# Kernel tuning notes

Measured on AMD Instinct MI355X. Metric: run time of the kernel, lower is better.

## Reference

```python
import jax, jax.numpy as jnp
import numpy as np

B, T, D = 8, 2048, 1024
FF = 4 * D
EPS = 1e-5


def setup_inputs() -> dict:
    key = jax.random.key(0)
    ks = jax.random.split(key, 20)
    rn = lambda k, s, sc=0.02: (jax.random.normal(k, s, jnp.float32) * sc)
    return {
        "x": jax.random.normal(ks[0], (B, T, D), jnp.float32),
        "ln1_g": jnp.ones((D,), jnp.float32),
        "ln1_b": jnp.zeros((D,), jnp.float32),
        "ln2_g": jnp.ones((D,), jnp.float32),
        "ln2_b": jnp.zeros((D,), jnp.float32),
        # time-mixing lerp coefficients in [0,1]
        "tm_mix_k": jax.random.uniform(ks[1], (D,), jnp.float32),
        "tm_mix_v": jax.random.uniform(ks[2], (D,), jnp.float32),
        "tm_mix_r": jax.random.uniform(ks[3], (D,), jnp.float32),
        # per-channel decay (log-log space, w = -exp(time_decay)) and first-token bonus
        "time_decay": rn(ks[4], (D,), 1.0),
        "time_first": rn(ks[5], (D,), 0.5),
        "wk": rn(ks[6], (D, D)),
        "wv": rn(ks[7], (D, D)),
        "wr": rn(ks[8], (D, D)),
        "wo": rn(ks[9], (D, D)),
        "cm_mix_k": jax.random.uniform(ks[10], (D,), jnp.float32),
        "cm_mix_r": jax.random.uniform(ks[11], (D,), jnp.float32),
        "cwk": rn(ks[12], (D, FF)),
        "cwv": rn(ks[13], (FF, D)),
        "cwr": rn(ks[14], (D, D)),
    }


def layer_norm(x, g, b):
    mu = jnp.mean(x, axis=-1, keepdims=True)
    var = jnp.var(x, axis=-1, keepdims=True)
    return (x - mu) * jax.lax.rsqrt(var + EPS) * g + b


def token_shift(x):
    # x[:, t-1] with zeros at t=0 (fresh state)
    return jnp.pad(x, ((0, 0), (1, 0), (0, 0)))[:, :-1]


def wkv_scan(k, v, time_decay, time_first):
    """Numerically-stable RWKV-4 WKV linear recurrence. k,v: [B,T,D]."""
    w = -jnp.exp(time_decay)  # [D], negative log-decay per step
    u = time_first

    def step(carry, kv):
        aa, bb, pp = carry  # each [B, D]
        kt, vt = kv
        ww = u + kt
        p = jnp.maximum(pp, ww)
        e1 = jnp.exp(pp - p)
        e2 = jnp.exp(ww - p)
        out = (e1 * aa + e2 * vt) / (e1 * bb + e2)
        ww2 = pp + w
        p2 = jnp.maximum(ww2, kt)
        e1b = jnp.exp(ww2 - p2)
        e2b = jnp.exp(kt - p2)
        return (e1b * aa + e2b * vt, e1b * bb + e2b, p2), out

    z = jnp.zeros((k.shape[0], k.shape[2]), k.dtype)
    init = (z, z, jnp.full_like(z, -1e38))
    _, outs = jax.lax.scan(step, init, (jnp.moveaxis(k, 1, 0), jnp.moveaxis(v, 1, 0)))
    return jnp.moveaxis(outs, 0, 1)  # [B,T,D]


def reference(x, ln1_g, ln1_b, ln2_g, ln2_b,
              tm_mix_k, tm_mix_v, tm_mix_r, time_decay, time_first,
              wk, wv, wr, wo, cm_mix_k, cm_mix_r, cwk, cwv, cwr):
    # --- Time mixing (pre-LN residual) ---
    h = layer_norm(x, ln1_g, ln1_b)
    hx = token_shift(h)
    k = jnp.einsum("btd,de->bte", h * tm_mix_k + hx * (1.0 - tm_mix_k), wk)
    v = jnp.einsum("btd,de->bte", h * tm_mix_v + hx * (1.0 - tm_mix_v), wv)
    r = jax.nn.sigmoid(jnp.einsum("btd,de->bte", h * tm_mix_r + hx * (1.0 - tm_mix_r), wr))
    wkv = wkv_scan(k, v, time_decay, time_first)
    x = x + jnp.einsum("btd,de->bte", r * wkv, wo)

    # --- Channel mixing (pre-LN residual) ---
    h = layer_norm(x, ln2_g, ln2_b)
    hx = token_shift(h)
    kk = jnp.einsum("btd,df->btf", h * cm_mix_k + hx * (1.0 - cm_mix_k), cwk)
    kk = jnp.square(jax.nn.relu(kk))  # [B,T,4D]
    rr = jax.nn.sigmoid(jnp.einsum("btd,de->bte", h * cm_mix_r + hx * (1.0 - cm_mix_r), cwr))
    x = x + rr * jnp.einsum("btf,fd->btd", kk, cwv)
    return x
```

## Files before the change

### kernel.cpp

```cpp
#include <hip/hip_runtime.h>

typedef unsigned short u16;
typedef float f32x4 __attribute__((ext_vector_type(4)));
typedef __bf16 bf16x8 __attribute__((ext_vector_type(8)));
typedef u16 u16x8 __attribute__((ext_vector_type(8)));
typedef u16 u16x4 __attribute__((ext_vector_type(4)));

static constexpr int D  = 1024;
static constexpr int T  = 2048;
static constexpr int NB = 8;
static constexpr int M  = NB * T;
static constexpr int FF = 4096;
static constexpr int NCH = 32;
static constexpr int CL  = T / NCH;

__device__ __forceinline__ u16 f2bf(float f) {
  unsigned u = __builtin_bit_cast(unsigned, f);
  return (u16)((u + 0x7fffu + ((u >> 16) & 1u)) >> 16);
}
__device__ __forceinline__ float bf2f(u16 s) {
  return __builtin_bit_cast(float, (unsigned)s << 16);
}

__device__ __forceinline__ void gload16(const u16* g, u16* l) {
  __builtin_amdgcn_global_load_lds(
      (const __attribute__((address_space(1))) void*)g,
      (__attribute__((address_space(3))) void*)l, 16, 0, 0);
}

__global__ __launch_bounds__(256) void ln_kernel(const float* __restrict__ x,
                                                 const float* __restrict__ g,
                                                 const float* __restrict__ b,
                                                 u16* __restrict__ h) {
  __shared__ float red[8];
  const int m = blockIdx.x;
  const int tid = threadIdx.x;
  const float* xr = x + (size_t)m * D;
  f32x4 v = *(const f32x4*)&xr[tid * 4];
  float s  = v[0] + v[1] + v[2] + v[3];
  float s2 = v[0]*v[0] + v[1]*v[1] + v[2]*v[2] + v[3]*v[3];
  #pragma unroll
  for (int o = 32; o > 0; o >>= 1) { s += __shfl_down(s, o); s2 += __shfl_down(s2, o); }
  if ((tid & 63) == 0) { red[tid >> 6] = s; red[4 + (tid >> 6)] = s2; }
  __syncthreads();
  s  = red[0] + red[1] + red[2] + red[3];
  s2 = red[4] + red[5] + red[6] + red[7];
  const float mu = s * (1.0f / D);
  const float rs = rsqrtf(s2 * (1.0f / D) - mu * mu + 1e-5f);
  u16x4 o4;
  #pragma unroll
  for (int i = 0; i < 4; ++i) {
    int d = tid * 4 + i;
    o4[i] = f2bf((v[i] - mu) * rs * g[d] + b[d]);
  }
  *(u16x4*)&h[(size_t)m * D + tid * 4] = o4;
}

__global__ __launch_bounds__(256) void mix3_kernel(const u16* __restrict__ h,
    const float* __restrict__ mk, const float* __restrict__ mv, const float* __restrict__ mr,
    u16* __restrict__ xk, u16* __restrict__ xv, u16* __restrict__ xr) {
  const int m = blockIdx.x;
  const int tid = threadIdx.x;
  const size_t base = (size_t)m * D + tid * 4;
  u16x4 hv = *(const u16x4*)&h[base];
  u16x4 hp = {0, 0, 0, 0};
  if ((m % T) != 0) hp = *(const u16x4*)&h[base - D];
  u16x4 ok, ov, orr;
  #pragma unroll
  for (int i = 0; i < 4; ++i) {
    int d = tid * 4 + i;
    float hc = bf2f(hv[i]), hx = bf2f(hp[i]);
    float a;
    a = mk[d]; ok[i]  = f2bf(hc * a + hx * (1.0f - a));
    a = mv[d]; ov[i]  = f2bf(hc * a + hx * (1.0f - a));
    a = mr[d]; orr[i] = f2bf(hc * a + hx * (1.0f - a));
  }
  *(u16x4*)&xk[base] = ok;
  *(u16x4*)&xv[base] = ov;
  *(u16x4*)&xr[base] = orr;
}

__global__ __launch_bounds__(256) void mix2_kernel(const u16* __restrict__ h,
    const float* __restrict__ mk, const float* __restrict__ mr,
    u16* __restrict__ xk, u16* __restrict__ xr) {
  const int m = blockIdx.x;
  const int tid = threadIdx.x;
  const size_t base = (size_t)m * D + tid * 4;
  u16x4 hv = *(const u16x4*)&h[base];
  u16x4 hp = {0, 0, 0, 0};
  if ((m % T) != 0) hp = *(const u16x4*)&h[base - D];
  u16x4 ok, orr;
  #pragma unroll
  for (int i = 0; i < 4; ++i) {
    int d = tid * 4 + i;
    float hc = bf2f(hv[i]), hx = bf2f(hp[i]);
    float a;
    a = mk[d]; ok[i]  = f2bf(hc * a + hx * (1.0f - a));
    a = mr[d]; orr[i] = f2bf(hc * a + hx * (1.0f - a));
  }
  *(u16x4*)&xk[base] = ok;
  *(u16x4*)&xr[base] = orr;
}

__global__ __launch_bounds__(256) void transpose_bf16_kernel(const float* __restrict__ in,
                                                             u16* __restrict__ out,
                                                             int K_, int N_) {
  __shared__ u16 t[32][33];
  const int k0 = blockIdx.x * 32, n0 = blockIdx.y * 32;
  const int r = threadIdx.x >> 5, c = threadIdx.x & 31;
  #pragma unroll
  for (int p = 0; p < 4; ++p)
    t[r + p * 8][c] = f2bf(in[(size_t)(k0 + r + p * 8) * N_ + n0 + c]);
  __syncthreads();
  #pragma unroll
  for (int p = 0; p < 4; ++p)
    out[(size_t)(n0 + r + p * 8) * K_ + k0 + c] = t[c][r + p * 8];
}

__global__ __launch_bounds__(256) void wkv_phase1(const float* __restrict__ K_,
                                                  const u16* __restrict__ V_,
                                                  const float* __restrict__ td,
                                                  float* __restrict__ aggA,
                                                  float* __restrict__ aggB,
                                                  float* __restrict__ aggP) {
  const int gid = blockIdx.x * 256 + threadIdx.x;
  const int d = gid & (D - 1);
  const int c = (gid >> 10) & (NCH - 1);
  const int b = gid >> 15;
  const float w = -expf(td[d]);
  float a = 0.0f, bb = 0.0f, p = -1e38f;
  size_t idx = ((size_t)b * T + (size_t)c * CL) * D + d;
  for (int t = 0; t < CL; ++t, idx += D) {
    const float kt = K_[idx];
    const float vt = bf2f(V_[idx]);
    const float wp = p + w;
    const float pn = fmaxf(wp, kt);
    const float e1 = expf(wp - pn), e2 = expf(kt - pn);
    a  = e1 * a  + e2 * vt;
    bb = e1 * bb + e2;
    p  = pn;
  }
  aggA[gid] = a; aggB[gid] = bb; aggP[gid] = p;
}

__global__ __launch_bounds__(256) void wkv_phase2(const float* __restrict__ td,
                                                  const float* __restrict__ aggA,
                                                  const float* __restrict__ aggB,
                                                  const float* __restrict__ aggP,
                                                  float* __restrict__ incA,
                                                  float* __restrict__ incB,
                                                  float* __restrict__ incP) {
  const int gid = blockIdx.x * 256 + threadIdx.x;
  const int d = gid & (D - 1);
  const int b = gid >> 10;
  const float cw = -expf(td[d]) * (float)CL;
  float a = 0.0f, bb = 0.0f, p = -1e38f;
  for (int c = 0; c < NCH; ++c) {
    const int i = (b * NCH + c) * D + d;
    incA[i] = a; incB[i] = bb; incP[i] = p;
    const float pd = p + cw;
    const float pc = aggP[i];
    const float pn = fmaxf(pd, pc);
    const float e1 = expf(pd - pn), e2 = expf(pc - pn);
    a  = e1 * a  + e2 * aggA[i];
    bb = e1 * bb + e2 * aggB[i];
    p  = pn;
  }
}

__global__ __launch_bounds__(256) void wkv_phase3(const float* __restrict__ K_,
                                                  const u16* __restrict__ V_,
                                                  const u16* __restrict__ R_,
                                                  const float* __restrict__ td,
                                                  const float* __restrict__ tf,
                                                  const float* __restrict__ incA,
                                                  const float* __restrict__ incB,
                                                  const float* __restrict__ incP,
                                                  u16* __restrict__ a2) {
  const int gid = blockIdx.x * 256 + threadIdx.x;
  const int d = gid & (D - 1);
  const int c = (gid >> 10) & (NCH - 1);
  const int b = gid >> 15;
  const float w = -expf(td[d]);
  const float u = tf[d];
  float aa = incA[gid], bb = incB[gid], pp = incP[gid];
  size_t idx = ((size_t)b * T + (size_t)c * CL) * D + d;
  for (int t = 0; t < CL; ++t, idx += D) {
    const float kt = K_[idx];
    const float vt = bf2f(V_[idx]);
    const float rt = bf2f(R_[idx]);
    const float ww = u + kt;
    const float p  = fmaxf(pp, ww);
    const float e1 = expf(pp - p), e2 = expf(ww - p);
    const float o  = (e1 * aa + e2 * vt) / (e1 * bb + e2);
    a2[idx] = f2bf(rt * o);
    const float ww2 = pp + w;
    const float p2  = fmaxf(ww2, kt);
    const float e1b = expf(ww2 - p2), e2b = expf(kt - p2);
    aa = e1b * aa + e2b * vt;
    bb = e1b * bb + e2b;
    pp = p2;
  }
}

template <int EPI>
__global__ __launch_bounds__(512, 2) void gemm8(const u16* __restrict__ A,
                                                const u16* __restrict__ Bt,
                                                int N, int K,
                                                float* __restrict__ outf,
                                                u16* __restrict__ outh,
                                                const float* __restrict__ auxf,
                                                const u16* __restrict__ auxh,
                                                float* __restrict__ dst) {
  __shared__ u16 sm[65536];
  const int m0 = blockIdx.x * 256;
  const int n0 = blockIdx.y * 256;
  const int tid = threadIdx.x;
  const int w = tid >> 6, l = tid & 63;
  const int wm = w >> 2, wn = w & 3;
  const int lr = l >> 3, ls = l & 7;
  const int NT = K >> 6;
  f32x4 acc[8][4] = {};

  const u16* gA = A + (size_t)(m0 + w * 8 + lr) * K + (ls ^ lr) * 8;
  const u16* gB = Bt + (size_t)(n0 + w * 8 + lr) * K + (ls ^ lr) * 8;

  auto stA = [&](int j, int r) {
    gload16(gA + ((size_t)r * 64) * K + (size_t)j * 64,
            &sm[(j & 1) * 16384 + (r * 64 + w * 8) * 64]);
  };
  auto stB = [&](int j, int r) {
    gload16(gB + ((size_t)r * 64) * K + (size_t)j * 64,
            &sm[32768 + (j & 1) * 16384 + (r * 64 + w * 8) * 64]);
  };

  stB(0, 0); stB(0, 1); stA(0, 0); stA(0, 2); stB(0, 2); stB(0, 3); stA(0, 1); stA(0, 3);
  if (1 < NT) {
    stB(1, 0); stB(1, 1); stA(1, 0); stA(1, 2); stB(1, 2); stB(1, 3);
    asm volatile("s_waitcnt vmcnt(6)" ::: "memory");
  } else {
    asm volatile("s_waitcnt vmcnt(0)" ::: "memory");
  }
  __builtin_amdgcn_s_barrier();

#define GEMM8_PHASE(Q, STAGE_CODE)                                          \
  {                                                                         \
    u16x8 aF[2][2];                                                         \
    _Pragma("unroll") for (int mi = 0; mi < 2; ++mi)                        \
      _Pragma("unroll") for (int ks = 0; ks < 2; ++ks) {                    \
        const int ra = wm * 128 + (Q) * 32 + mi * 16 + (l & 15);            \
        const int rs = ks * 4 + (l >> 4);                                   \
        aF[mi][ks] = *(const u16x8*)&sA[ra * 64 + ((rs ^ (ra & 7)) * 8)];   \
      }                                                                     \
    STAGE_CODE;                                                             \
    __builtin_amdgcn_s_barrier();                                           \
    asm volatile("s_waitcnt lgkmcnt(0)" ::: "memory");                      \
    __builtin_amdgcn_sched_barrier(0);                                      \
    __builtin_amdgcn_s_setprio(1);                                          \
    _Pragma("unroll") for (int ks = 0; ks < 2; ++ks)                        \
      _Pragma("unroll") for (int mi = 0; mi < 2; ++mi)                      \
        _Pragma("unroll") for (int ni = 0; ni < 4; ++ni)                    \
          acc[(Q) * 2 + mi][ni] = __builtin_amdgcn_mfma_f32_16x16x32_bf16(  \
              __builtin_bit_cast(bf16x8, aF[mi][ks]),                       \
              __builtin_bit_cast(bf16x8, bF[ni][ks]),                       \
              acc[(Q) * 2 + mi][ni], 0, 0, 0);                              \
    __builtin_amdgcn_s_setprio(0);                                          \
  }

  for (int k = 0; k < NT; ++k) {
    const u16* sA = &sm[(k & 1) * 16384];
    const u16* sB = &sm[32768 + (k & 1) * 16384];
    u16x8 bF[4][2];
    #pragma unroll
    for (int ni = 0; ni < 4; ++ni)
      #pragma unroll
      for (int ks = 0; ks < 2; ++ks) {
        const int rb = wn * 64 + ni * 16 + (l & 15);
        const int rs = ks * 4 + (l >> 4);
        bF[ni][ks] = *(const u16x8*)&sB[rb * 64 + ((rs ^ (rb & 7)) * 8)];
      }
    GEMM8_PHASE(0, if (k + 1 < NT) { stA(k + 1, 1); stA(k + 1, 3); })
    __builtin_amdgcn_s_barrier();
    GEMM8_PHASE(1, if (k + 2 < NT) { stB(k + 2, 0); stB(k + 2, 1); })
    __builtin_amdgcn_s_barrier();
    GEMM8_PHASE(2, if (k + 2 < NT) { stA(k + 2, 0); stA(k + 2, 2); })
    __builtin_amdgcn_s_barrier();
    GEMM8_PHASE(3, if (k + 2 < NT) { stB(k + 2, 2); stB(k + 2, 3); })
    if (k + 2 < NT) asm volatile("s_waitcnt vmcnt(6)" ::: "memory");
    else            asm volatile("s_waitcnt vmcnt(0)" ::: "memory");
    __builtin_amdgcn_s_barrier();
  }
#undef GEMM8_PHASE

  const int cl = l & 15, rh = l >> 4;
  #pragma unroll
  for (int mi = 0; mi < 8; ++mi) {
    #pragma unroll
    for (int ni = 0; ni < 4; ++ni) {
      const int gn = n0 + wn * 64 + ni * 16 + cl;
      #pragma unroll
      for (int j = 0; j < 4; ++j) {
        const int gm = m0 + wm * 128 + mi * 16 + rh * 4 + j;
        const float c = acc[mi][ni][j];
        const size_t o = (size_t)gm * N + gn;
        if (EPI == 0) outf[o] = c;
        else if (EPI == 1) outh[o] = f2bf(1.0f / (1.0f + expf(-c)));
        else if (EPI == 2) outf[o] = auxf[o] + c;
        else if (EPI == 3) { const float t = c > 0.0f ? c : 0.0f; outh[o] = f2bf(t * t); }
        else if (EPI == 4) dst[o] += bf2f(auxh[o]) * c;
        else if (EPI == 5) outh[o] = f2bf(c);
      }
    }
  }
}

extern "C" void kernel_launch(void* const* d_in, const int* in_sizes, int n_in,
                              void* d_out, int out_size, void* d_ws, size_t ws_size,
                              hipStream_t stream) {
  (void)in_sizes; (void)n_in; (void)out_size;
  const float* x      = (const float*)d_in[0];
  const float* ln1_g  = (const float*)d_in[1];
  const float* ln1_b  = (const float*)d_in[2];
  const float* ln2_g  = (const float*)d_in[3];
  const float* ln2_b  = (const float*)d_in[4];
  const float* tm_k   = (const float*)d_in[5];
  const float* tm_v   = (const float*)d_in[6];
  const float* tm_r   = (const float*)d_in[7];
  const float* tdec   = (const float*)d_in[8];
  const float* tfir   = (const float*)d_in[9];
  const float* wk     = (const float*)d_in[10];
  const float* wv     = (const float*)d_in[11];
  const float* wr     = (const float*)d_in[12];
  const float* wo     = (const float*)d_in[13];
  const float* cm_k   = (const float*)d_in[14];
  const float* cm_r   = (const float*)d_in[15];
  const float* cwk    = (const float*)d_in[16];
  const float* cwv    = (const float*)d_in[17];
  const float* cwr    = (const float*)d_in[18];
  float* out = (float*)d_out;

  const size_t MB = 1024 * 1024;
  if (ws_size < 218 * MB) return;

  char* w = (char*)d_ws;
  u16*   h    = (u16*)(w);
  u16*   b32  = (u16*)(w + 32 * MB);
  u16*   b64  = (u16*)(w + 64 * MB);
  u16*   b96  = (u16*)(w + 96 * MB);
  float* Kf   = (float*)(w + 128 * MB);
  u16*   KK   = (u16*)(w + 64 * MB);
  u16*   wkT  = (u16*)(w + 192 * MB);
  u16*   wvT  = (u16*)(w + 194 * MB);
  u16*   wrT  = (u16*)(w + 196 * MB);
  u16*   woT  = (u16*)(w + 198 * MB);
  u16*   cwkT = (u16*)(w + 200 * MB);
  u16*   cwvT = (u16*)(w + 208 * MB);
  u16*   cwrT = (u16*)(w + 216 * MB);
  float* aggA = (float*)(w + 96 * MB);
  float* aggB = (float*)(w + 97 * MB);
  float* aggP = (float*)(w + 98 * MB);
  float* incA = (float*)(w + 99 * MB);
  float* incB = (float*)(w + 100 * MB);
  float* incP = (float*)(w + 101 * MB);

  transpose_bf16_kernel<<<dim3(D / 32, D / 32), 256, 0, stream>>>(wk, wkT, D, D);
  transpose_bf16_kernel<<<dim3(D / 32, D / 32), 256, 0, stream>>>(wv, wvT, D, D);
  transpose_bf16_kernel<<<dim3(D / 32, D / 32), 256, 0, stream>>>(wr, wrT, D, D);
  transpose_bf16_kernel<<<dim3(D / 32, D / 32), 256, 0, stream>>>(wo, woT, D, D);
  transpose_bf16_kernel<<<dim3(D / 32, FF / 32), 256, 0, stream>>>(cwk, cwkT, D, FF);
  transpose_bf16_kernel<<<dim3(FF / 32, D / 32), 256, 0, stream>>>(cwv, cwvT, FF, D);
  transpose_bf16_kernel<<<dim3(D / 32, D / 32), 256, 0, stream>>>(cwr, cwrT, D, D);

  ln_kernel<<<M, 256, 0, stream>>>(x, ln1_g, ln1_b, h);
  mix3_kernel<<<M, 256, 0, stream>>>(h, tm_k, tm_v, tm_r, b32, b64, b96);

  dim3 gD(M / 256, D / 256);
  gemm8<0><<<gD, 512, 0, stream>>>(b32, wkT, D, D, Kf, nullptr, nullptr, nullptr, nullptr);
  gemm8<5><<<gD, 512, 0, stream>>>(b64, wvT, D, D, nullptr, b32, nullptr, nullptr, nullptr);
  gemm8<1><<<gD, 512, 0, stream>>>(b96, wrT, D, D, nullptr, h, nullptr, nullptr, nullptr);

  wkv_phase1<<<(NB * NCH * D) / 256, 256, 0, stream>>>(Kf, b32, tdec, aggA, aggB, aggP);
  wkv_phase2<<<(NB * D) / 256, 256, 0, stream>>>(tdec, aggA, aggB, aggP, incA, incB, incP);
  wkv_phase3<<<(NB * NCH * D) / 256, 256, 0, stream>>>(Kf, b32, h, tdec, tfir,
                                                       incA, incB, incP, b64);

  gemm8<2><<<gD, 512, 0, stream>>>(b64, woT, D, D, out, nullptr, x, nullptr, nullptr);

  ln_kernel<<<M, 256, 0, stream>>>(out, ln2_g, ln2_b, h);
  mix2_kernel<<<M, 256, 0, stream>>>(h, cm_k, cm_r, b32, b64);

  gemm8<1><<<gD, 512, 0, stream>>>(b64, cwrT, D, D, nullptr, h, nullptr, nullptr, nullptr);

  dim3 gF(M / 256, FF / 256);
  gemm8<3><<<gF, 512, 0, stream>>>(b32, cwkT, FF, D, nullptr, KK, nullptr, nullptr, nullptr);

  dim3 gO(M / 256, D / 256);
  gemm8<4><<<gO, 512, 0, stream>>>(KK, cwvT, D, FF, nullptr, nullptr, nullptr, h, out);
}
```

Measured before the change: 722.8 us.

## Double-buffer LDS fragment loads in GEMM and remap blocks per XCD

Changes the GEMM main loop so the A fragments for the next quarter-phase, and the B fragments plus first A fragment for the next K tile, are loaded from LDS while the current MFMAs run. This removes the explicit lgkmcnt wait before each MFMA group. It also remaps the block index so consecutive M tiles go to the same XCD, aiming for better L2 reuse. The cost is higher register pressure from the extra fragment buffers, and the reordered vmcnt waits plus barriers risk LDS hazards.

```diff
diff --git a/kernel.cpp b/kernel.cpp
--- a/kernel.cpp
+++ b/kernel.cpp
@@ -213,8 +213,12 @@
                                                 const u16* __restrict__ auxh,
                                                 float* __restrict__ dst) {
   __shared__ u16 sm[65536];
-  const int m0 = blockIdx.x * 256;
-  const int n0 = blockIdx.y * 256;
+  const int gx = gridDim.x, gy = gridDim.y;
+  const int fid = blockIdx.y * gx + blockIdx.x;
+  const int xcd = fid & 7, sl = fid >> 3;
+  const int m0 = (xcd * (gx >> 3) + sl / gy) * 256;
+  const int n0 = (sl % gy) * 256;
+
   const int tid = threadIdx.x;
   const int w = tid >> 6, l = tid & 63;
   const int wm = w >> 2, wn = w & 3;
@@ -234,43 +238,9 @@
             &sm[32768 + (j & 1) * 16384 + (r * 64 + w * 8) * 64]);
   };
 
-  stB(0, 0); stB(0, 1); stA(0, 0); stA(0, 2); stB(0, 2); stB(0, 3); stA(0, 1); stA(0, 3);
-  if (1 < NT) {
-    stB(1, 0); stB(1, 1); stA(1, 0); stA(1, 2); stB(1, 2); stB(1, 3);
-    asm volatile("s_waitcnt vmcnt(6)" ::: "memory");
-  } else {
-    asm volatile("s_waitcnt vmcnt(0)" ::: "memory");
-  }
-  __builtin_amdgcn_s_barrier();
-
-#define GEMM8_PHASE(Q, STAGE_CODE)                                          \
-  {                                                                         \
-    u16x8 aF[2][2];                                                         \
-    _Pragma("unroll") for (int mi = 0; mi < 2; ++mi)                        \
-      _Pragma("unroll") for (int ks = 0; ks < 2; ++ks) {                    \
-        const int ra = wm * 128 + (Q) * 32 + mi * 16 + (l & 15);            \
-        const int rs = ks * 4 + (l >> 4);                                   \
-        aF[mi][ks] = *(const u16x8*)&sA[ra * 64 + ((rs ^ (ra & 7)) * 8)];   \
-      }                                                                     \
-    STAGE_CODE;                                                             \
-    __builtin_amdgcn_s_barrier();                                           \
-    asm volatile("s_waitcnt lgkmcnt(0)" ::: "memory");                      \
-    __builtin_amdgcn_sched_barrier(0);                                      \
-    __builtin_amdgcn_s_setprio(1);                                          \
-    _Pragma("unroll") for (int ks = 0; ks < 2; ++ks)                        \
-      _Pragma("unroll") for (int mi = 0; mi < 2; ++mi)                      \
-        _Pragma("unroll") for (int ni = 0; ni < 4; ++ni)                    \
-          acc[(Q) * 2 + mi][ni] = __builtin_amdgcn_mfma_f32_16x16x32_bf16(  \
-              __builtin_bit_cast(bf16x8, aF[mi][ks]),                       \
-              __builtin_bit_cast(bf16x8, bF[ni][ks]),                       \
-              acc[(Q) * 2 + mi][ni], 0, 0, 0);                              \
-    __builtin_amdgcn_s_setprio(0);                                          \
-  }
-
-  for (int k = 0; k < NT; ++k) {
-    const u16* sA = &sm[(k & 1) * 16384];
-    const u16* sB = &sm[32768 + (k & 1) * 16384];
-    u16x8 bF[4][2];
+  u16x8 bF[4][2], aA[2][2], aB[2][2];
+
+  auto ldB8 = [&](const u16* sB) {
     #pragma unroll
     for (int ni = 0; ni < 4; ++ni)
       #pragma unroll
@@ -279,18 +249,67 @@
         const int rs = ks * 4 + (l >> 4);
         bF[ni][ks] = *(const u16x8*)&sB[rb * 64 + ((rs ^ (rb & 7)) * 8)];
       }
-    GEMM8_PHASE(0, if (k + 1 < NT) { stA(k + 1, 1); stA(k + 1, 3); })
-    __builtin_amdgcn_s_barrier();
-    GEMM8_PHASE(1, if (k + 2 < NT) { stB(k + 2, 0); stB(k + 2, 1); })
-    __builtin_amdgcn_s_barrier();
-    GEMM8_PHASE(2, if (k + 2 < NT) { stA(k + 2, 0); stA(k + 2, 2); })
-    __builtin_amdgcn_s_barrier();
-    GEMM8_PHASE(3, if (k + 2 < NT) { stB(k + 2, 2); stB(k + 2, 3); })
-    if (k + 2 < NT) asm volatile("s_waitcnt vmcnt(6)" ::: "memory");
+  };
+
+#define LDA(q, dstf, sAp)                                                   \
+  _Pragma("unroll") for (int mi = 0; mi < 2; ++mi)                          \
+    _Pragma("unroll") for (int ks = 0; ks < 2; ++ks) {                      \
+      const int ra = wm * 128 + (q) * 32 + mi * 16 + (l & 15);              \
+      const int rs = ks * 4 + (l >> 4);                                     \
+      dstf[mi][ks] = *(const u16x8*)&sAp[ra * 64 + ((rs ^ (ra & 7)) * 8)];  \
+    }
+
+#define MFMA16(Q, srcf)                                                     \
+  __builtin_amdgcn_s_setprio(1);                                            \
+  _Pragma("unroll") for (int ks = 0; ks < 2; ++ks)                          \
+    _Pragma("unroll") for (int mi = 0; mi < 2; ++mi)                        \
+      _Pragma("unroll") for (int ni = 0; ni < 4; ++ni)                      \
+        acc[(Q) * 2 + mi][ni] = __builtin_amdgcn_mfma_f32_16x16x32_bf16(    \
+            __builtin_bit_cast(bf16x8, srcf[mi][ks]),                       \
+            __builtin_bit_cast(bf16x8, bF[ni][ks]),                         \
+            acc[(Q) * 2 + mi][ni], 0, 0, 0);                                \
+  __builtin_amdgcn_s_setprio(0);
+
+  stB(0, 0); stB(0, 1); stA(0, 0); stA(0, 2); stB(0, 2); stB(0, 3); stA(0, 1); stA(0, 3);
+  if (1 < NT) {
+    stB(1, 0); stB(1, 1); stA(1, 0); stA(1, 2); stB(1, 2); stB(1, 3);
+    asm volatile("s_waitcnt vmcnt(6)" ::: "memory");
+  } else {
+    asm volatile("s_waitcnt vmcnt(0)" ::: "memory");
+  }
+  __builtin_amdgcn_s_barrier();
+  ldB8(&sm[32768]);
+  LDA(0, aA, (&sm[0]));
+
+  for (int k = 0; k < NT; ++k) {
+    const u16* sA  = &sm[(k & 1) * 16384];
+    const u16* sAn = &sm[((k + 1) & 1) * 16384];
+    const u16* sBn = &sm[32768 + ((k + 1) & 1) * 16384];
+    LDA(1, aB, sA);
+    if (k + 1 < NT) { stA(k + 1, 1); stA(k + 1, 3); }
+    __builtin_amdgcn_s_barrier();
+    MFMA16(0, aA);
+    __builtin_amdgcn_s_barrier();
+    LDA(2, aA, sA);
+    if (k + 2 < NT) { stB(k + 2, 0); stB(k + 2, 1); }
+    __builtin_amdgcn_s_barrier();
+    MFMA16(1, aB);
+    __builtin_amdgcn_s_barrier();
+    if (k + 2 < NT) asm volatile("s_waitcnt vmcnt(2)" ::: "memory");
     else            asm volatile("s_waitcnt vmcnt(0)" ::: "memory");
-    __builtin_amdgcn_s_barrier();
-  }
-#undef GEMM8_PHASE
+    LDA(3, aB, sA);
+    if (k + 2 < NT) { stA(k + 2, 0); stA(k + 2, 2); }
+    __builtin_amdgcn_s_barrier();
+    MFMA16(2, aA);
+    __builtin_amdgcn_s_barrier();
+    if (k + 2 < NT) { stB(k + 2, 2); stB(k + 2, 3); }
+    __builtin_amdgcn_s_barrier();
+    MFMA16(3, aB);
+    if (k + 1 < NT) { ldB8(sBn); LDA(0, aA, sAn); }
+    __builtin_amdgcn_s_barrier();
+  }
+#undef LDA
+#undef MFMA16
 
   const int cl = l & 15, rh = l >> 4;
   #pragma unroll
```

After: 719.3 us. About the same (-0.5%).
